# Kernel optimization log

Measured on AMD Instinct MI355X. Metric: run time of the kernel, lower is better.

Reference implementation:

```python
import jax, jax.numpy as jnp
import numpy as np

H = 512  # hidden_size


def setup_inputs() -> dict:
    key = jax.random.key(0)
    ks = jax.random.split(key, 8)
    B, L_tgt, L_src = 4, 32, 1024
    query = jax.random.normal(ks[0], (B, L_tgt, H), dtype=jnp.float32)
    states = jax.random.normal(ks[1], (B, L_src, 2 * H), dtype=jnp.float32)
    source_mask = jnp.ones((B, L_src), dtype=jnp.int32)
    s = 0.02
    Wq = jax.random.normal(ks[2], (H, 2 * H), dtype=jnp.float32) * s      # _linear_query.weight^T
    bq = jax.random.normal(ks[3], (2 * H,), dtype=jnp.float32) * s        # _linear_query.bias
    Ws = jax.random.normal(ks[4], (2 * H, 2 * H), dtype=jnp.float32) * s  # _linear_source.weight^T (no bias)
    v = jax.random.normal(ks[5], (2 * H,), dtype=jnp.float32) * s         # _v.weight (no bias)
    Wc = jax.random.normal(ks[6], (3 * H, H), dtype=jnp.float32) * s      # _context.weight^T
    bc = jax.random.normal(ks[7], (H,), dtype=jnp.float32) * s            # _context.bias
    return {"query": query, "states": states, "source_mask": source_mask,
            "Wq": Wq, "bq": bq, "Ws": Ws, "v": v, "Wc": Wc, "bc": bc}


def reference(query, states, source_mask, Wq, bq, Ws, v, Wc, bc):
    # Bahdanau additive attention.
    # query: (B, T, H), states: (B, S, 2H), source_mask: (B, S)
    qf = query @ Wq + bq                         # (B, T, 2H)
    sf = states @ Ws                             # (B, S, 2H)
    # alignments: v . tanh(qf[:, :, None] + sf[:, None, :])  -> (B, T, S)
    feats = jnp.tanh(qf[:, :, None, :] + sf[:, None, :, :])  # (B, T, S, 2H)
    alignments = jnp.einsum('btsd,d->bts', feats, v)
    # mask (B, S) -> (B, 1, S); masked positions get -inf before softmax
    alignments = jnp.where(source_mask[:, None, :].astype(bool), alignments, -jnp.inf)
    attentions = jax.nn.softmax(alignments, axis=2)           # (B, T, S)
    context = jnp.einsum('bts,bsd->btd', attentions, states)  # (B, T, 2H)
    concat_context = jnp.concatenate((context, query), axis=2)  # (B, T, 3H)
    attention_hidden = concat_context @ Wc + bc               # (B, T, H)
    attentions_t = jnp.swapaxes(attentions, 1, 2)             # (B, S, T)
    return (context, attention_hidden, attentions_t)
```

## Files before the change

### kernel.cpp

```cpp
#include <hip/hip_runtime.h>
#include <math.h>


typedef unsigned short u16;
typedef __bf16 bf16x8 __attribute__((ext_vector_type(8)));
typedef float floatx4 __attribute__((ext_vector_type(4)));

#define B_ 4
#define T_ 32
#define S_ 1024
#define H_ 512
#define D_ 1024
#define BT_ 128
#define TWO_LOG2E 2.8853900817779268f
#define LOG2E 1.4426950408889634f

__device__ __forceinline__ float bf2f(u16 u) {
  unsigned int i = ((unsigned int)u) << 16;
  return __builtin_bit_cast(float, i);
}
__device__ __forceinline__ u16 f2bf(float f) {
  unsigned int i = __builtin_bit_cast(unsigned int, f);
  i += 0x7fffu + ((i >> 16) & 1u);
  return (u16)(i >> 16);
}
__device__ __forceinline__ void ld_g2l_16(const u16* g, u16* l) {
  __builtin_amdgcn_global_load_lds((__attribute__((address_space(1))) void*)(u16*)g,
                                   (__attribute__((address_space(3))) void*)l, 16, 0, 0);
}


__global__ __launch_bounds__(256) void prep_fused6(const float* __restrict__ states, const float* __restrict__ Ws,
                                                   const float* __restrict__ query, const float* __restrict__ Wq,
                                                   const float* __restrict__ bq,
                                                   const float* __restrict__ Wc, const float* __restrict__ bc,
                                                   u16* __restrict__ sbf, u16* __restrict__ sbfT,
                                                   u16* __restrict__ WsT, float* __restrict__ qfp,
                                                   float* __restrict__ rowsum, float* __restrict__ hid) {
  __shared__ u16 tile[32][65];
  __shared__ float q[8][128];
  const int t = threadIdx.x;
  if (blockIdx.x < 256) {
    const int idx = blockIdx.x;
    const int c0 = (idx & 3) * 256, r0 = ((idx >> 2) & 15) * 8, ks = idx >> 6;
    const int k0 = ks * 128;
    for (int i = t; i < 8 * 128; i += 256) {
      const int rl = i >> 7, kk = i & 127;
      q[rl][kk] = query[(size_t)(r0 + rl) * H_ + k0 + kk];
    }
    __syncthreads();
    const int col = c0 + t;
    float acc[8] = {};
    for (int kk = 0; kk < 128; ++kk) {
      const float w = Wq[(size_t)(k0 + kk) * D_ + col];
#pragma unroll
      for (int r = 0; r < 8; ++r) acc[r] = fmaf(q[r][kk], w, acc[r]);
    }
    const float bb = (ks == 0) ? bq[col] : 0.f;
    float* dst = qfp + (size_t)ks * (BT_ * D_);
#pragma unroll
    for (int r = 0; r < 8; ++r)
      dst[(size_t)(r0 + r) * D_ + col] = TWO_LOG2E * (acc[r] + bb);
  } else if (blockIdx.x < 384) {
    const int idx = blockIdx.x - 256;
    const int c0 = (idx & 1) * 256, r0 = ((idx >> 1) & 15) * 8, ks = idx >> 5;
    const int k0 = ks * 128;
    for (int i = t; i < 8 * 128; i += 256) {
      const int rl = i >> 7, kk = i & 127;
      q[rl][kk] = query[(size_t)(r0 + rl) * H_ + k0 + kk];
    }
    __syncthreads();
    const int col = c0 + t;
    float acc[8] = {};
    for (int kk = 0; kk < 128; ++kk) {
      const float w = Wc[(size_t)(D_ + k0 + kk) * H_ + col];
#pragma unroll
      for (int r = 0; r < 8; ++r) acc[r] = fmaf(q[r][kk], w, acc[r]);
    }
    const float bb = (ks == 0) ? bc[col] : 0.f;
#pragma unroll
    for (int r = 0; r < 8; ++r)
      atomicAdd(&hid[(size_t)(r0 + r) * H_ + col], acc[r] + bb);
  } else if (blockIdx.x < 896) {
    const int bid = blockIdx.x - 384;
    if (bid == 0 && t < 128) rowsum[t] = 0.f;
    const int n0 = (bid & 15) * 64, k0 = (bid >> 4) * 32;
    const int kr = t >> 3, nc = (t & 7) * 8;
    const float* p = Ws + (size_t)(k0 + kr) * D_ + n0 + nc;
    float4 a = *(const float4*)p, b = *(const float4*)(p + 4);
    tile[kr][nc + 0] = f2bf(a.x); tile[kr][nc + 1] = f2bf(a.y);
    tile[kr][nc + 2] = f2bf(a.z); tile[kr][nc + 3] = f2bf(a.w);
    tile[kr][nc + 4] = f2bf(b.x); tile[kr][nc + 5] = f2bf(b.y);
    tile[kr][nc + 6] = f2bf(b.z); tile[kr][nc + 7] = f2bf(b.w);
    __syncthreads();
    const int nr = t >> 2, kc = (t & 3) * 8;
    union { uint4 v; u16 s[8]; } st;
#pragma unroll
    for (int i = 0; i < 8; ++i) st.s[i] = tile[kc + i][nr];
    *(uint4*)(WsT + (size_t)(n0 + nr) * D_ + k0 + kc) = st.v;
  } else {
    const int bid = blockIdx.x - 896;
    const int b = bid >> 9;
    const int r2 = bid & 511;
    const int d0 = (r2 & 15) * 64, s0 = (r2 >> 4) * 32;
    const int sr = t >> 3, dc = (t & 7) * 8;
    const float* p = states + ((size_t)b * S_ + s0 + sr) * D_ + d0 + dc;
    float4 a = *(const float4*)p, bb = *(const float4*)(p + 4);
    union { uint4 v; u16 s[8]; } pk;
    pk.s[0] = f2bf(a.x); pk.s[1] = f2bf(a.y); pk.s[2] = f2bf(a.z); pk.s[3] = f2bf(a.w);
    pk.s[4] = f2bf(bb.x); pk.s[5] = f2bf(bb.y); pk.s[6] = f2bf(bb.z); pk.s[7] = f2bf(bb.w);
    *(uint4*)(sbf + ((size_t)b * S_ + s0 + sr) * D_ + d0 + dc) = pk.v;
#pragma unroll
    for (int i = 0; i < 8; ++i) tile[sr][dc + i] = pk.s[i];
    __syncthreads();
    const int dr = t >> 2, sc = (t & 3) * 8;
    union { uint4 v; u16 s[8]; } st;
#pragma unroll
    for (int i = 0; i < 8; ++i) st.s[i] = tile[sc + i][dr];
    *(uint4*)(sbfT + ((size_t)b * D_ + d0 + dr) * S_ + s0 + sc) = st.v;
  }
}

__device__ __forceinline__ void f2f_stage(const u16* __restrict__ A, const u16* __restrict__ BT,
                                          u16* sAb, u16* sBb, int bm0, int bn0, int k0,
                                          int wv, int srow, int sp) {
#pragma unroll
  for (int j = 0; j < 4; ++j) {
    const int r = wv * 32 + j * 8 + srow;
    const int c = sp ^ (r & 7);
    ld_g2l_16(A + (size_t)(bm0 + r) * D_ + k0 + c * 8, sAb + (wv * 32 + j * 8) * 64);
  }
#pragma unroll
  for (int j = 0; j < 2; ++j) {
    const int r = wv * 16 + j * 8 + srow;
    const int c = sp ^ (r & 7);
    ld_g2l_16(BT + (size_t)(bn0 + r) * D_ + k0 + c * 8, sBb + (wv * 16 + j * 8) * 64);
  }
}

__device__ __forceinline__ void f2f_compute(const u16* sAb, const u16* sBb,
                                            int wm, int wn, int fm, int fq, floatx4 (&acc)[4][2]) {
#pragma unroll
  for (int win = 0; win < 2; ++win) {
    bf16x8 af[4], bfr[2];
#pragma unroll
    for (int i = 0; i < 4; ++i) {
      const int R = wm + i * 16 + fm;
      af[i] = *(const bf16x8*)&sAb[R * 64 + ((win * 4 + fq) ^ (R & 7)) * 8];
    }
#pragma unroll
    for (int j = 0; j < 2; ++j) {
      const int R = wn + j * 16 + fm;
      bfr[j] = *(const bf16x8*)&sBb[R * 64 + ((win * 4 + fq) ^ (R & 7)) * 8];
    }
#pragma unroll
    for (int i = 0; i < 4; ++i)
#pragma unroll
      for (int j = 0; j < 2; ++j)
        acc[i][j] = __builtin_amdgcn_mfma_f32_16x16x32_bf16(af[i], bfr[j], acc[i][j], 0, 0, 0);
  }
}

__global__ __launch_bounds__(256) void f2i_sfgemm(const u16* __restrict__ A, const u16* __restrict__ BT,
                                                  const float* __restrict__ qfp, float* __restrict__ Eq,
                                                  u16* __restrict__ Es) {
  __shared__ __align__(16) u16 sA[2][128 * 64];
  __shared__ __align__(16) u16 sB[2][64 * 64];
  const int bm0 = blockIdx.y * 128, bn0 = blockIdx.x * 64;
  const int t = threadIdx.x;
  const int wv = t >> 6, lane = t & 63;
  const int wm = (wv >> 1) * 64, wn = (wv & 1) * 32;
  const int fm = lane & 15, fq = lane >> 4;
  const int srow = lane >> 3, sp = lane & 7;

  {
    const int bid = blockIdx.y * 16 + blockIdx.x;
    const int idx = bid * 256 + t;
    const float s = qfp[idx] + qfp[BT_ * D_ + idx] +
                    qfp[2 * BT_ * D_ + idx] + qfp[3 * BT_ * D_ + idx];
    Eq[idx] = __builtin_amdgcn_exp2f(s);
  }

  floatx4 acc[4][2];
  const floatx4 fz = {0.f, 0.f, 0.f, 0.f};
#pragma unroll
  for (int i = 0; i < 4; ++i) { acc[i][0] = fz; acc[i][1] = fz; }

  f2f_stage(A, BT, sA[0], sB[0], bm0, bn0, 0, wv, srow, sp);
#pragma unroll 1
  for (int k0 = 0; k0 < D_; k0 += 128) {
    f2f_stage(A, BT, sA[1], sB[1], bm0, bn0, k0 + 64, wv, srow, sp);
    asm volatile("s_waitcnt vmcnt(6)" ::: "memory");
    __builtin_amdgcn_s_barrier();
    f2f_compute(sA[0], sB[0], wm, wn, fm, fq, acc);
    __builtin_amdgcn_s_barrier();
    if (k0 + 128 < D_) {
      f2f_stage(A, BT, sA[0], sB[0], bm0, bn0, k0 + 128, wv, srow, sp);
      asm volatile("s_waitcnt vmcnt(6)" ::: "memory");
    } else {
      asm volatile("s_waitcnt vmcnt(0)" ::: "memory");
    }
    __builtin_amdgcn_s_barrier();
    f2f_compute(sA[1], sB[1], wm, wn, fm, fq, acc);
    __builtin_amdgcn_s_barrier();
  }
#pragma unroll
  for (int i = 0; i < 4; ++i)
#pragma unroll
    for (int j = 0; j < 2; ++j)
#pragma unroll
      for (int r = 0; r < 4; ++r) {
        const int row = bm0 + wm + i * 16 + fq * 4 + r;
        const int col = bn0 + wn + j * 16 + fm;
        Es[(size_t)row * D_ + col] = f2bf(__builtin_amdgcn_exp2f(TWO_LOG2E * acc[i][j][r]));
      }
}

__global__ __launch_bounds__(256) void f3k_align(const float* __restrict__ Eq, const u16* __restrict__ Es,
                                                 const float* __restrict__ v, const int* __restrict__ mask,
                                                 u16* __restrict__ pbf, float* __restrict__ rowsum) {
  __shared__ float red[32][4];
  const int wv = threadIdx.x >> 6, lane = threadIdx.x & 63;
  const int w = blockIdx.x * 4 + wv;
  const int b = w >> 8;
  const int s0 = (w & 255) * 4;
  const int m0 = mask[(size_t)b * S_ + s0 + 0];
  const int m1 = mask[(size_t)b * S_ + s0 + 1];
  const int m2 = mask[(size_t)b * S_ + s0 + 2];
  const int m3 = mask[(size_t)b * S_ + s0 + 3];
  float vm2[16], es0[16], es1[16], es2[16], es3[16];
  float sumv = 0.f;
  {
    union { uint4 u[2]; u16 h[16]; } u0, u1, u2, u3;
    const uint4* ep0 = (const uint4*)(Es + ((size_t)b * S_ + s0 + 0) * D_ + lane * 16);
    const uint4* ep1 = (const uint4*)(Es + ((size_t)b * S_ + s0 + 1) * D_ + lane * 16);
    const uint4* ep2 = (const uint4*)(Es + ((size_t)b * S_ + s0 + 2) * D_ + lane * 16);
    const uint4* ep3 = (const uint4*)(Es + ((size_t)b * S_ + s0 + 3) * D_ + lane * 16);
    u0.u[0] = ep0[0]; u0.u[1] = ep0[1];
    u1.u[0] = ep1[0]; u1.u[1] = ep1[1];
    u2.u[0] = ep2[0]; u2.u[1] = ep2[1];
    u3.u[0] = ep3[0]; u3.u[1] = ep3[1];
    const float4* vp = (const float4*)(v + lane * 16);
#pragma unroll
    for (int c = 0; c < 4; ++c) {
      const float4 w4 = vp[c];
      vm2[4 * c + 0] = -2.f * w4.x; vm2[4 * c + 1] = -2.f * w4.y;
      vm2[4 * c + 2] = -2.f * w4.z; vm2[4 * c + 3] = -2.f * w4.w;
      sumv += w4.x + w4.y + w4.z + w4.w;
    }
#pragma unroll
    for (int j = 0; j < 16; ++j) {
      es0[j] = bf2f(u0.h[j]); es1[j] = bf2f(u1.h[j]);
      es2[j] = bf2f(u2.h[j]); es3[j] = bf2f(u3.h[j]);
    }
  }
  const float* qbase = Eq + ((size_t)(b * T_)) * D_ + lane * 16;
  for (int tc = 0; tc < 8; ++tc) {
    float sa[4], sb[4], sc[4], sd[4];
#pragma unroll
    for (int ti = 0; ti < 4; ++ti) {
      const float4* qp = (const float4*)(qbase + (size_t)(tc * 4 + ti) * D_);
      float a0 = sumv, a1 = sumv, a2 = sumv, a3 = sumv;
#pragma unroll
      for (int c = 0; c < 4; ++c) {
        const float4 q4 = qp[c];
        const float xs[4] = {q4.x, q4.y, q4.z, q4.w};
#pragma unroll
        for (int u2 = 0; u2 < 4; ++u2) {
          const int j = 4 * c + u2;
          a0 = fmaf(vm2[j], __builtin_amdgcn_rcpf(fmaf(xs[u2], es0[j], 1.f)), a0);
          a1 = fmaf(vm2[j], __builtin_amdgcn_rcpf(fmaf(xs[u2], es1[j], 1.f)), a1);
          a2 = fmaf(vm2[j], __builtin_amdgcn_rcpf(fmaf(xs[u2], es2[j], 1.f)), a2);
          a3 = fmaf(vm2[j], __builtin_amdgcn_rcpf(fmaf(xs[u2], es3[j], 1.f)), a3);
        }
      }
      sa[ti] = a0; sb[ti] = a1; sc[ti] = a2; sd[ti] = a3;
    }
#pragma unroll
    for (int off = 32; off > 0; off >>= 1)
#pragma unroll
      for (int ti = 0; ti < 4; ++ti) {
        sa[ti] += __shfl_xor(sa[ti], off);
        sb[ti] += __shfl_xor(sb[ti], off);
        sc[ti] += __shfl_xor(sc[ti], off);
        sd[ti] += __shfl_xor(sd[ti], off);
      }
    if (lane == 0) {
#pragma unroll
      for (int ti = 0; ti < 4; ++ti) {
        const int tt = tc * 4 + ti;
        const float e0 = m0 ? __builtin_amdgcn_exp2f(sa[ti] * LOG2E) : 0.f;
        const float e1 = m1 ? __builtin_amdgcn_exp2f(sb[ti] * LOG2E) : 0.f;
        const float e2 = m2 ? __builtin_amdgcn_exp2f(sc[ti] * LOG2E) : 0.f;
        const float e3 = m3 ? __builtin_amdgcn_exp2f(sd[ti] * LOG2E) : 0.f;
        const u16 p0 = f2bf(e0), p1 = f2bf(e1), p2 = f2bf(e2), p3 = f2bf(e3);
        uint2 pk;
        pk.x = (unsigned int)p0 | ((unsigned int)p1 << 16);
        pk.y = (unsigned int)p2 | ((unsigned int)p3 << 16);
        *(uint2*)&pbf[((size_t)(b * T_ + tt)) * S_ + s0] = pk;
        red[tt][wv] = bf2f(p0) + bf2f(p1) + bf2f(p2) + bf2f(p3);
      }
    }
  }
  __syncthreads();
  if (threadIdx.x < 32) {
    const int bb = blockIdx.x >> 6;
    const float rs = red[threadIdx.x][0] + red[threadIdx.x][1] +
                     red[threadIdx.x][2] + red[threadIdx.x][3];
    atomicAdd(&rowsum[bb * 32 + threadIdx.x], rs);
  }
}

__global__ __launch_bounds__(256) void f5e_context(const u16* __restrict__ pbf, const u16* __restrict__ sbfT,
                                                   const float* __restrict__ rowsum,
                                                   float* __restrict__ ctx, float* __restrict__ out_at) {
  __shared__ float rinv[32];
  __shared__ float red[4][64][9];
  const int b = blockIdx.x >> 6, dt = blockIdx.x & 63;
  const int wv = threadIdx.x >> 6, lane = threadIdx.x & 63;
  if (threadIdx.x < 32) rinv[threadIdx.x] = 1.f / rowsum[b * 32 + threadIdx.x];
  const int n0 = dt * 16;
  const int fm = lane & 15, fq = lane >> 4;
  const floatx4 fz = {0.f, 0.f, 0.f, 0.f};
  floatx4 acc0 = fz, acc1 = fz;
  const u16* pa0 = pbf + ((size_t)b * T_ + fm) * S_ + wv * 256 + fq * 8;
  const u16* pa1 = pa0 + (size_t)16 * S_;
  const u16* pb  = sbfT + ((size_t)b * D_ + n0 + fm) * S_ + wv * 256 + fq * 8;
#pragma unroll
  for (int k0 = 0; k0 < 256; k0 += 32) {
    bf16x8 a0 = *(const bf16x8*)(pa0 + k0);
    bf16x8 a1 = *(const bf16x8*)(pa1 + k0);
    bf16x8 bb = *(const bf16x8*)(pb + k0);
    acc0 = __builtin_amdgcn_mfma_f32_16x16x32_bf16(a0, bb, acc0, 0, 0, 0);
    acc1 = __builtin_amdgcn_mfma_f32_16x16x32_bf16(a1, bb, acc1, 0, 0, 0);
  }
#pragma unroll
  for (int r = 0; r < 4; ++r) {
    red[wv][lane][r] = acc0[r];
    red[wv][lane][4 + r] = acc1[r];
  }
  __syncthreads();
  const int s0a = dt * 16;
  for (int i = threadIdx.x; i < 512; i += 256) {
    const int tt = i & 31, sl = i >> 5;
    const float e = bf2f(pbf[((size_t)(b * T_ + tt)) * S_ + s0a + sl]);
    out_at[((size_t)(b * S_ + s0a + sl)) * T_ + tt] = e * rinv[tt];
  }
  if (wv == 0) {
#pragma unroll
    for (int r = 0; r < 4; ++r) {
      const float v0 = red[0][lane][r] + red[1][lane][r] + red[2][lane][r] + red[3][lane][r];
      const float v1 = red[0][lane][4 + r] + red[1][lane][4 + r] +
                       red[2][lane][4 + r] + red[3][lane][4 + r];
      const int t0r = fq * 4 + r;
      ctx[((size_t)b * T_ + t0r) * D_ + n0 + fm] = v0 * rinv[t0r];
      ctx[((size_t)b * T_ + 16 + t0r) * D_ + n0 + fm] = v1 * rinv[16 + t0r];
    }
  }
}

__global__ __launch_bounds__(256) void f6c_outproj(const float* __restrict__ ctx,
                                                   const float* __restrict__ Wc,
                                                   float* __restrict__ out_hid) {
  __shared__ float cq[16][128];
  const int c0 = blockIdx.x * 128, r0 = blockIdx.y * 16, k0 = blockIdx.z * 128;
  const int tid = threadIdx.x;
  const int cl = tid & 127, rh = tid >> 7;
  for (int i = tid; i < 16 * 128; i += 256) {
    const int rl = i >> 7, kk = i & 127;
    cq[rl][kk] = ctx[(size_t)(r0 + rl) * D_ + k0 + kk];
  }
  __syncthreads();
  float acc[8] = {};
  for (int kk = 0; kk < 128; ++kk) {
    const float w = Wc[(size_t)(k0 + kk) * H_ + c0 + cl];
#pragma unroll
    for (int rr = 0; rr < 8; ++rr) acc[rr] = fmaf(cq[rh * 8 + rr][kk], w, acc[rr]);
  }
#pragma unroll
  for (int rr = 0; rr < 8; ++rr)
    atomicAdd(&out_hid[(size_t)(r0 + rh * 8 + rr) * H_ + c0 + cl], acc[rr]);
}


__global__ __launch_bounds__(256) void prep_fused(const float* __restrict__ states, const float* __restrict__ Ws,
                                                  const float* __restrict__ query, const float* __restrict__ Wq,
                                                  const float* __restrict__ bq,
                                                  u16* __restrict__ sbf, u16* __restrict__ sbfT,
                                                  u16* __restrict__ WsT, float* __restrict__ qf) {
  __shared__ u16 tile[32][65];
  __shared__ float q[8][128];
  const int t = threadIdx.x;
  if (blockIdx.x < 512) {
    const int n0 = (blockIdx.x & 15) * 64, k0 = (blockIdx.x >> 4) * 32;
    const int kr = t >> 3, nc = (t & 7) * 8;
    const float* p = Ws + (size_t)(k0 + kr) * D_ + n0 + nc;
    float4 a = *(const float4*)p, b = *(const float4*)(p + 4);
    tile[kr][nc + 0] = f2bf(a.x); tile[kr][nc + 1] = f2bf(a.y);
    tile[kr][nc + 2] = f2bf(a.z); tile[kr][nc + 3] = f2bf(a.w);
    tile[kr][nc + 4] = f2bf(b.x); tile[kr][nc + 5] = f2bf(b.y);
    tile[kr][nc + 6] = f2bf(b.z); tile[kr][nc + 7] = f2bf(b.w);
    __syncthreads();
    const int nr = t >> 2, kc = (t & 3) * 8;
    union { uint4 v; u16 s[8]; } st;
#pragma unroll
    for (int i = 0; i < 8; ++i) st.s[i] = tile[kc + i][nr];
    *(uint4*)(WsT + (size_t)(n0 + nr) * D_ + k0 + kc) = st.v;
  } else if (blockIdx.x < 2560) {
    const int bid = blockIdx.x - 512;
    const int b = bid >> 9;
    const int r2 = bid & 511;
    const int d0 = (r2 & 15) * 64, s0 = (r2 >> 4) * 32;
    const int sr = t >> 3, dc = (t & 7) * 8;
    const float* p = states + ((size_t)b * S_ + s0 + sr) * D_ + d0 + dc;
    float4 a = *(const float4*)p, bb = *(const float4*)(p + 4);
    union { uint4 v; u16 s[8]; } pk;
    pk.s[0] = f2bf(a.x); pk.s[1] = f2bf(a.y); pk.s[2] = f2bf(a.z); pk.s[3] = f2bf(a.w);
    pk.s[4] = f2bf(bb.x); pk.s[5] = f2bf(bb.y); pk.s[6] = f2bf(bb.z); pk.s[7] = f2bf(bb.w);
    *(uint4*)(sbf + ((size_t)b * S_ + s0 + sr) * D_ + d0 + dc) = pk.v;
#pragma unroll
    for (int i = 0; i < 8; ++i) tile[sr][dc + i] = pk.s[i];
    __syncthreads();
    const int dr = t >> 2, sc = (t & 3) * 8;
    union { uint4 v; u16 s[8]; } st;
#pragma unroll
    for (int i = 0; i < 8; ++i) st.s[i] = tile[sc + i][dr];
    *(uint4*)(sbfT + ((size_t)b * D_ + d0 + dr) * S_ + s0 + sc) = st.v;
  } else {
    const int idx = blockIdx.x - 2560;
    const int c0 = (idx & 3) * 256, r0 = ((idx >> 2) & 15) * 8, k0 = (idx >> 6) * 128;
    for (int i = t; i < 8 * 128; i += 256) {
      const int rl = i >> 7, kk = i & 127;
      q[rl][kk] = query[(size_t)(r0 + rl) * H_ + k0 + kk];
    }
    __syncthreads();
    const int col = c0 + t;
    float acc[8] = {};
    for (int kk = 0; kk < 128; ++kk) {
      const float w = Wq[(size_t)(k0 + kk) * D_ + col];
#pragma unroll
      for (int r = 0; r < 8; ++r) acc[r] = fmaf(q[r][kk], w, acc[r]);
    }
    const float bb = (k0 == 0) ? bq[col] : 0.f;
#pragma unroll
    for (int r = 0; r < 8; ++r)
      atomicAdd(&qf[(size_t)(r0 + r) * D_ + col], TWO_LOG2E * (acc[r] + bb));
  }
}

__global__ __launch_bounds__(256) void f2e_sfgemm(const u16* __restrict__ A, const u16* __restrict__ BT,
                                                  u16* __restrict__ Cb) {
  __shared__ __align__(16) u16 sA[128 * 64];
  __shared__ __align__(16) u16 sB[64 * 64];
  const int bm0 = blockIdx.y * 128, bn0 = blockIdx.x * 64;
  const int t = threadIdx.x;
  const int wv = t >> 6, lane = t & 63;
  const int wm = (wv >> 1) * 64, wn = (wv & 1) * 32;
  const int fm = lane & 15, fq = lane >> 4;
  const int srow = lane >> 3, sp = lane & 7;

  floatx4 acc[4][2];
  const floatx4 fz = {0.f, 0.f, 0.f, 0.f};
#pragma unroll
  for (int i = 0; i < 4; ++i) { acc[i][0] = fz; acc[i][1] = fz; }

  for (int k0 = 0; k0 < D_; k0 += 64) {
    __syncthreads();
#pragma unroll
    for (int j = 0; j < 4; ++j) {
      const int r = wv * 32 + j * 8 + srow;
      const int c = sp ^ (r & 7);
      ld_g2l_16(A + (size_t)(bm0 + r) * D_ + k0 + c * 8, &sA[(wv * 32 + j * 8) * 64]);
    }
#pragma unroll
    for (int j = 0; j < 2; ++j) {
      const int r = wv * 16 + j * 8 + srow;
      const int c = sp ^ (r & 7);
      ld_g2l_16(BT + (size_t)(bn0 + r) * D_ + k0 + c * 8, &sB[(wv * 16 + j * 8) * 64]);
    }
    __syncthreads();
#pragma unroll
    for (int win = 0; win < 2; ++win) {
      bf16x8 af[4], bfr[2];
#pragma unroll
      for (int i = 0; i < 4; ++i) {
        const int R = wm + i * 16 + fm;
        af[i] = *(const bf16x8*)&sA[R * 64 + ((win * 4 + fq) ^ (R & 7)) * 8];
      }
#pragma unroll
      for (int j = 0; j < 2; ++j) {
        const int R = wn + j * 16 + fm;
        bfr[j] = *(const bf16x8*)&sB[R * 64 + ((win * 4 + fq) ^ (R & 7)) * 8];
      }
#pragma unroll
      for (int i = 0; i < 4; ++i)
#pragma unroll
        for (int j = 0; j < 2; ++j)
          acc[i][j] = __builtin_amdgcn_mfma_f32_16x16x32_bf16(af[i], bfr[j], acc[i][j], 0, 0, 0);
    }
  }
#pragma unroll
  for (int i = 0; i < 4; ++i)
#pragma unroll
    for (int j = 0; j < 2; ++j)
#pragma unroll
      for (int r = 0; r < 4; ++r) {
        const int row = bm0 + wm + i * 16 + fq * 4 + r;
        const int col = bn0 + wn + j * 16 + fm;
        Cb[(size_t)row * D_ + col] = f2bf(TWO_LOG2E * acc[i][j][r]);
      }
}

__global__ __launch_bounds__(256, 6) void f3f_align(const float* __restrict__ qf, const u16* __restrict__ sfb,
                                                    const float* __restrict__ v, float* __restrict__ alg) {
  const int wid = (blockIdx.x * 256 + threadIdx.x) >> 6;
  const int lane = threadIdx.x & 63;
  const int b = wid >> 10, s = wid & 1023;
  const int t0 = blockIdx.y * 16;
  float vr[16], sr[16];
  {
    union { uint4 v[2]; u16 s[16]; } u;
    const uint4* sp = (const uint4*)(sfb + (size_t)wid * D_ + lane * 16);
    u.v[0] = sp[0]; u.v[1] = sp[1];
    const float* vp = v + lane * 16;
#pragma unroll
    for (int c = 0; c < 4; ++c) {
      float4 w = *(const float4*)(vp + 4 * c);
      vr[4 * c + 0] = w.x; vr[4 * c + 1] = w.y; vr[4 * c + 2] = w.z; vr[4 * c + 3] = w.w;
    }
#pragma unroll
    for (int j = 0; j < 16; ++j) sr[j] = bf2f(u.s[j]);
  }
  float sum[16];
#pragma unroll
  for (int tt = 0; tt < 16; ++tt) sum[tt] = 0.f;

  const float* qbase = qf + ((size_t)(b * T_ + t0)) * D_ + lane * 16;
  for (int tt = 0; tt < 16; ++tt) {
    const float4* qp = (const float4*)(qbase + (size_t)tt * D_);
    float acc = 0.f;
#pragma unroll
    for (int c = 0; c < 4; ++c) {
      float4 q4 = qp[c];
      float xs[4] = {q4.x, q4.y, q4.z, q4.w};
#pragma unroll
      for (int u2 = 0; u2 < 4; ++u2) {
        const int j = 4 * c + u2;
        const float x = xs[u2] + sr[j];
        const float e = __builtin_amdgcn_exp2f(x);
        acc = fmaf(vr[j], fmaf(-2.f, __builtin_amdgcn_rcpf(e + 1.f), 1.f), acc);
      }
    }
    sum[tt] = acc;
  }
#pragma unroll
  for (int off = 32; off > 0; off >>= 1)
#pragma unroll
    for (int tt = 0; tt < 16; ++tt) sum[tt] += __shfl_xor(sum[tt], off);
  if (lane == 0) {
#pragma unroll
    for (int tt = 0; tt < 16; ++tt)
      alg[((size_t)(b * T_ + t0 + tt)) * S_ + s] = sum[tt];
  }
}

__global__ __launch_bounds__(256) void f4b_softmax(const float* __restrict__ alg, const int* __restrict__ mask,
                                                   float* __restrict__ out_at, u16* __restrict__ pbf) {
  const int r = blockIdx.x;
  const int b = r >> 5, t = r & 31;
  const int tid = threadIdx.x;
  __shared__ float red[256];
  float a[4];
#pragma unroll
  for (int jj = 0; jj < 4; ++jj) {
    const int s = tid + 256 * jj;
    const float x = alg[(size_t)r * S_ + s];
    a[jj] = (mask[(size_t)b * S_ + s] != 0) ? x : -3.0e38f;
  }
  float m = fmaxf(fmaxf(a[0], a[1]), fmaxf(a[2], a[3]));
  red[tid] = m; __syncthreads();
  for (int st = 128; st > 0; st >>= 1) { if (tid < st) red[tid] = fmaxf(red[tid], red[tid + st]); __syncthreads(); }
  m = red[0]; __syncthreads();
  float e[4], lsum = 0.f;
#pragma unroll
  for (int jj = 0; jj < 4; ++jj) {
    e[jj] = (a[jj] > -1.0e38f) ? expf(a[jj] - m) : 0.f;
    lsum += e[jj];
  }
  red[tid] = lsum; __syncthreads();
  for (int st = 128; st > 0; st >>= 1) { if (tid < st) red[tid] += red[tid + st]; __syncthreads(); }
  const float rs = 1.f / red[0];
#pragma unroll
  for (int jj = 0; jj < 4; ++jj) {
    const int s = tid + 256 * jj;
    const float p = e[jj] * rs;
    out_at[((size_t)b * S_ + s) * T_ + t] = p;
    pbf[(size_t)r * S_ + s] = f2bf(p);
  }
}

__global__ __launch_bounds__(256) void f5c_context(const u16* __restrict__ pbf, const u16* __restrict__ sbfT,
                                                   float* __restrict__ ctx) {
  const int b = blockIdx.x >> 4, dt = blockIdx.x & 15;
  const int wv = threadIdx.x >> 6, lane = threadIdx.x & 63;
  const int n0 = dt * 64 + wv * 16;
  const int fm = lane & 15, fq = lane >> 4;
  const floatx4 fz = {0.f, 0.f, 0.f, 0.f};
  floatx4 acc0 = fz, acc1 = fz;
  const u16* pa0 = pbf + ((size_t)b * T_ + fm) * S_ + fq * 8;
  const u16* pa1 = pbf + ((size_t)b * T_ + 16 + fm) * S_ + fq * 8;
  const u16* pb  = sbfT + ((size_t)b * D_ + n0 + fm) * S_ + fq * 8;
#pragma unroll 4
  for (int k0 = 0; k0 < S_; k0 += 32) {
    bf16x8 a0 = *(const bf16x8*)(pa0 + k0);
    bf16x8 a1 = *(const bf16x8*)(pa1 + k0);
    bf16x8 bb = *(const bf16x8*)(pb + k0);
    acc0 = __builtin_amdgcn_mfma_f32_16x16x32_bf16(a0, bb, acc0, 0, 0, 0);
    acc1 = __builtin_amdgcn_mfma_f32_16x16x32_bf16(a1, bb, acc1, 0, 0, 0);
  }
  const int col = n0 + fm;
#pragma unroll
  for (int r = 0; r < 4; ++r) {
    ctx[((size_t)b * T_ + fq * 4 + r) * D_ + col] = acc0[r];
    ctx[((size_t)b * T_ + 16 + fq * 4 + r) * D_ + col] = acc1[r];
  }
}

__global__ __launch_bounds__(256) void f6b_outproj(const float* __restrict__ ctx, const float* __restrict__ query,
                                                   const float* __restrict__ Wc, const float* __restrict__ bc,
                                                   float* __restrict__ out_hid) {
  __shared__ float cq[16][128];
  const int c0 = blockIdx.x * 128, r0 = blockIdx.y * 16, k0 = blockIdx.z * 128;
  const int tid = threadIdx.x;
  const int cl = tid & 127, rh = tid >> 7;
  for (int i = tid; i < 16 * 128; i += 256) {
    const int rl = i >> 7, kk = i & 127;
    const int k = k0 + kk, row = r0 + rl;
    cq[rl][kk] = (k < D_) ? ctx[(size_t)row * D_ + k] : query[(size_t)row * H_ + k - D_];
  }
  __syncthreads();
  float acc[8] = {};
  for (int kk = 0; kk < 128; ++kk) {
    const float w = Wc[(size_t)(k0 + kk) * H_ + c0 + cl];
#pragma unroll
    for (int rr = 0; rr < 8; ++rr) acc[rr] = fmaf(cq[rh * 8 + rr][kk], w, acc[rr]);
  }
  const float bb = (blockIdx.z == 0) ? bc[c0 + cl] : 0.f;
#pragma unroll
  for (int rr = 0; rr < 8; ++rr)
    atomicAdd(&out_hid[(size_t)(r0 + rh * 8 + rr) * H_ + c0 + cl], acc[rr] + bb);
}


__global__ __launch_bounds__(256) void kc_cvt(const float* __restrict__ in, u16* __restrict__ out) {
  const size_t i0 = ((size_t)blockIdx.x * 256 + threadIdx.x) * 8;
  float4 a = *(const float4*)(in + i0);
  float4 b = *(const float4*)(in + i0 + 4);
  union { uint4 v; u16 s[8]; } r;
  r.s[0] = f2bf(a.x); r.s[1] = f2bf(a.y); r.s[2] = f2bf(a.z); r.s[3] = f2bf(a.w);
  r.s[4] = f2bf(b.x); r.s[5] = f2bf(b.y); r.s[6] = f2bf(b.z); r.s[7] = f2bf(b.w);
  *(uint4*)(out + i0) = r.v;
}

__global__ __launch_bounds__(256) void f0_transpose(const float* __restrict__ Ws, u16* __restrict__ WsT) {
  __shared__ u16 tile[32][65];
  const int n0 = blockIdx.x * 64, k0 = blockIdx.y * 32;
  const int t = threadIdx.x;
  {
    const int kr = t >> 3, nc = (t & 7) * 8;
    const float* p = Ws + (size_t)(k0 + kr) * D_ + n0 + nc;
    float4 a = *(const float4*)p, b = *(const float4*)(p + 4);
    tile[kr][nc + 0] = f2bf(a.x); tile[kr][nc + 1] = f2bf(a.y);
    tile[kr][nc + 2] = f2bf(a.z); tile[kr][nc + 3] = f2bf(a.w);
    tile[kr][nc + 4] = f2bf(b.x); tile[kr][nc + 5] = f2bf(b.y);
    tile[kr][nc + 6] = f2bf(b.z); tile[kr][nc + 7] = f2bf(b.w);
  }
  __syncthreads();
  {
    const int nr = t >> 2, kc = (t & 3) * 8;
    union { uint4 v; u16 s[8]; } st;
#pragma unroll
    for (int i = 0; i < 8; ++i) st.s[i] = tile[kc + i][nr];
    *(uint4*)(WsT + (size_t)(n0 + nr) * D_ + k0 + kc) = st.v;
  }
}

__global__ __launch_bounds__(256) void f1b_qf(const float* __restrict__ query, const float* __restrict__ Wq,
                                              const float* __restrict__ bq, float* __restrict__ qf) {
  __shared__ float q[8][128];
  const int c0 = blockIdx.x * 256, r0 = blockIdx.y * 8, k0 = blockIdx.z * 128;
  const int tid = threadIdx.x;
  for (int i = tid; i < 8 * 128; i += 256) {
    const int rl = i >> 7, kk = i & 127;
    q[rl][kk] = query[(size_t)(r0 + rl) * H_ + k0 + kk];
  }
  __syncthreads();
  const int col = c0 + tid;
  float acc[8] = {};
  for (int kk = 0; kk < 128; ++kk) {
    const float w = Wq[(size_t)(k0 + kk) * D_ + col];
#pragma unroll
    for (int r = 0; r < 8; ++r) acc[r] = fmaf(q[r][kk], w, acc[r]);
  }
  const float bb = (blockIdx.z == 0) ? bq[col] : 0.f;
#pragma unroll
  for (int r = 0; r < 8; ++r)
    atomicAdd(&qf[(size_t)(r0 + r) * D_ + col], TWO_LOG2E * (acc[r] + bb));
}

__global__ __launch_bounds__(256) void f2c_sfgemm(const u16* __restrict__ A, const u16* __restrict__ BT,
                                                  u16* __restrict__ Cb) {
  __shared__ __align__(16) u16 sA[128 * 40];
  __shared__ __align__(16) u16 sB[64 * 40];
  const int bm0 = blockIdx.y * 128, bn0 = blockIdx.x * 64;
  const int t = threadIdx.x;
  const int wv = t >> 6, lane = t & 63;
  const int wm = (wv >> 1) * 64, wn = (wv & 1) * 32;
  const int fm = lane & 15, fq = lane >> 4;
  const int arow = t >> 1, akc = (t & 1) * 16;
  const int brow = t >> 2, bkc = (t & 3) * 8;
  floatx4 acc[4][2];
  const floatx4 fz = {0.f, 0.f, 0.f, 0.f};
#pragma unroll
  for (int i = 0; i < 4; ++i) { acc[i][0] = fz; acc[i][1] = fz; }
  const uint4* gA = (const uint4*)(A + (size_t)(bm0 + arow) * D_ + akc);
  const uint4* gB = (const uint4*)(BT + (size_t)(bn0 + brow) * D_ + bkc);
  for (int k0 = 0; k0 < D_; k0 += 32) {
    uint4 va0 = gA[k0 >> 3];
    uint4 va1 = gA[(k0 >> 3) + 1];
    uint4 vb = gB[k0 >> 3];
    __syncthreads();
    *(uint4*)&sA[arow * 40 + akc] = va0;
    *(uint4*)&sA[arow * 40 + akc + 8] = va1;
    *(uint4*)&sB[brow * 40 + bkc] = vb;
    __syncthreads();
    bf16x8 af[4], bfr[2];
#pragma unroll
    for (int i = 0; i < 4; ++i) af[i] = *(const bf16x8*)&sA[(wm + i * 16 + fm) * 40 + fq * 8];
#pragma unroll
    for (int j = 0; j < 2; ++j) bfr[j] = *(const bf16x8*)&sB[(wn + j * 16 + fm) * 40 + fq * 8];
#pragma unroll
    for (int i = 0; i < 4; ++i)
#pragma unroll
      for (int j = 0; j < 2; ++j)
        acc[i][j] = __builtin_amdgcn_mfma_f32_16x16x32_bf16(af[i], bfr[j], acc[i][j], 0, 0, 0);
  }
#pragma unroll
  for (int i = 0; i < 4; ++i)
#pragma unroll
    for (int j = 0; j < 2; ++j)
#pragma unroll
      for (int r = 0; r < 4; ++r) {
        const int row = bm0 + wm + i * 16 + fq * 4 + r;
        const int col = bn0 + wn + j * 16 + fm;
        Cb[(size_t)row * D_ + col] = f2bf(TWO_LOG2E * acc[i][j][r]);
      }
}

__global__ __launch_bounds__(256) void f2d_sfgemm(const float* __restrict__ A, const u16* __restrict__ BT,
                                                  u16* __restrict__ Cb) {
  __shared__ __align__(16) u16 sA[128 * 40];
  __shared__ __align__(16) u16 sB[64 * 40];
  const int bm0 = blockIdx.y * 128, bn0 = blockIdx.x * 64;
  const int t = threadIdx.x;
  const int wv = t >> 6, lane = t & 63;
  const int wm = (wv >> 1) * 64, wn = (wv & 1) * 32;
  const int fm = lane & 15, fq = lane >> 4;
  const int arow = t >> 1, akc = (t & 1) * 16;
  const int brow = t >> 2, bkc = (t & 3) * 8;
  floatx4 acc[4][2];
  const floatx4 fz = {0.f, 0.f, 0.f, 0.f};
#pragma unroll
  for (int i = 0; i < 4; ++i) { acc[i][0] = fz; acc[i][1] = fz; }
  const float* gA = A + (size_t)(bm0 + arow) * D_ + akc;
  const uint4* gB = (const uint4*)(BT + (size_t)(bn0 + brow) * D_ + bkc);
  for (int k0 = 0; k0 < D_; k0 += 32) {
    float4 a0 = *(const float4*)(gA + k0);
    float4 a1 = *(const float4*)(gA + k0 + 4);
    float4 a2 = *(const float4*)(gA + k0 + 8);
    float4 a3 = *(const float4*)(gA + k0 + 12);
    uint4 vb = gB[k0 >> 3];
    union { uint4 v[2]; u16 s[16]; } pa;
    pa.s[0] = f2bf(a0.x); pa.s[1] = f2bf(a0.y); pa.s[2] = f2bf(a0.z); pa.s[3] = f2bf(a0.w);
    pa.s[4] = f2bf(a1.x); pa.s[5] = f2bf(a1.y); pa.s[6] = f2bf(a1.z); pa.s[7] = f2bf(a1.w);
    pa.s[8] = f2bf(a2.x); pa.s[9] = f2bf(a2.y); pa.s[10] = f2bf(a2.z); pa.s[11] = f2bf(a2.w);
    pa.s[12] = f2bf(a3.x); pa.s[13] = f2bf(a3.y); pa.s[14] = f2bf(a3.z); pa.s[15] = f2bf(a3.w);
    __syncthreads();
    *(uint4*)&sA[arow * 40 + akc] = pa.v[0];
    *(uint4*)&sA[arow * 40 + akc + 8] = pa.v[1];
    *(uint4*)&sB[brow * 40 + bkc] = vb;
    __syncthreads();
    bf16x8 af[4], bfr[2];
#pragma unroll
    for (int i = 0; i < 4; ++i) af[i] = *(const bf16x8*)&sA[(wm + i * 16 + fm) * 40 + fq * 8];
#pragma unroll
    for (int j = 0; j < 2; ++j) bfr[j] = *(const bf16x8*)&sB[(wn + j * 16 + fm) * 40 + fq * 8];
#pragma unroll
    for (int i = 0; i < 4; ++i)
#pragma unroll
      for (int j = 0; j < 2; ++j)
        acc[i][j] = __builtin_amdgcn_mfma_f32_16x16x32_bf16(af[i], bfr[j], acc[i][j], 0, 0, 0);
  }
#pragma unroll
  for (int i = 0; i < 4; ++i)
#pragma unroll
    for (int j = 0; j < 2; ++j)
#pragma unroll
      for (int r = 0; r < 4; ++r) {
        const int row = bm0 + wm + i * 16 + fq * 4 + r;
        const int col = bn0 + wn + j * 16 + fm;
        Cb[(size_t)row * D_ + col] = f2bf(TWO_LOG2E * acc[i][j][r]);
      }
}

__global__ __launch_bounds__(256) void f4_softmax(const float* __restrict__ alg, const int* __restrict__ mask,
                                                  float* __restrict__ attn) {
  const int r = blockIdx.x;
  const int b = r >> 5;
  const int tid = threadIdx.x;
  __shared__ float red[256];
  float a[4];
#pragma unroll
  for (int jj = 0; jj < 4; ++jj) {
    const int s = tid + 256 * jj;
    const float x = alg[(size_t)r * S_ + s];
    a[jj] = (mask[(size_t)b * S_ + s] != 0) ? x : -3.0e38f;
  }
  float m = fmaxf(fmaxf(a[0], a[1]), fmaxf(a[2], a[3]));
  red[tid] = m; __syncthreads();
  for (int st = 128; st > 0; st >>= 1) { if (tid < st) red[tid] = fmaxf(red[tid], red[tid + st]); __syncthreads(); }
  m = red[0]; __syncthreads();
  float e[4], lsum = 0.f;
#pragma unroll
  for (int jj = 0; jj < 4; ++jj) {
    e[jj] = (a[jj] > -1.0e38f) ? expf(a[jj] - m) : 0.f;
    lsum += e[jj];
  }
  red[tid] = lsum; __syncthreads();
  for (int st = 128; st > 0; st >>= 1) { if (tid < st) red[tid] += red[tid + st]; __syncthreads(); }
  const float rs = 1.f / red[0];
#pragma unroll
  for (int jj = 0; jj < 4; ++jj)
    attn[(size_t)r * S_ + tid + 256 * jj] = e[jj] * rs;
}

__global__ __launch_bounds__(256) void f5b_context(const float* __restrict__ attn, const u16* __restrict__ sbf,
                                                   float* __restrict__ ctx, float* __restrict__ out_at) {
  __shared__ float at[16][64];
  const int s0 = blockIdx.x * 64, t0 = blockIdx.y * 16, b = blockIdx.z;
  const int tid = threadIdx.x;
  for (int i = tid; i < 16 * 64; i += 256) {
    const int tl = i >> 6, sl = i & 63;
    at[tl][sl] = attn[(size_t)(b * T_ + t0 + tl) * S_ + s0 + sl];
  }
  __syncthreads();
  for (int i = tid; i < 64 * 16; i += 256) {
    const int sl = i >> 4, tl = i & 15;
    out_at[((size_t)b * S_ + s0 + sl) * T_ + t0 + tl] = at[tl][sl];
  }
  float acc[16][4] = {};
  for (int sl = 0; sl < 64; ++sl) {
    const u16* srow = sbf + ((size_t)b * S_ + s0 + sl) * D_ + tid;
    float sv[4];
#pragma unroll
    for (int jj = 0; jj < 4; ++jj) sv[jj] = bf2f(srow[256 * jj]);
#pragma unroll
    for (int tl = 0; tl < 16; ++tl) {
      const float w = at[tl][sl];
#pragma unroll
      for (int jj = 0; jj < 4; ++jj) acc[tl][jj] = fmaf(w, sv[jj], acc[tl][jj]);
    }
  }
#pragma unroll
  for (int tl = 0; tl < 16; ++tl)
#pragma unroll
    for (int jj = 0; jj < 4; ++jj)
      atomicAdd(&ctx[(size_t)(b * T_ + t0 + tl) * D_ + tid + 256 * jj], acc[tl][jj]);
}

__global__ __launch_bounds__(256) void f5_context(const float* __restrict__ attn, const float* __restrict__ states,
                                                  float* __restrict__ ctx, float* __restrict__ out_at) {
  __shared__ float at[16][64];
  const int s0 = blockIdx.x * 64, t0 = blockIdx.y * 16, b = blockIdx.z;
  const int tid = threadIdx.x;
  for (int i = tid; i < 16 * 64; i += 256) {
    const int tl = i >> 6, sl = i & 63;
    at[tl][sl] = attn[(size_t)(b * T_ + t0 + tl) * S_ + s0 + sl];
  }
  __syncthreads();
  for (int i = tid; i < 64 * 16; i += 256) {
    const int sl = i >> 4, tl = i & 15;
    out_at[((size_t)b * S_ + s0 + sl) * T_ + t0 + tl] = at[tl][sl];
  }
  float acc[16][4] = {};
  for (int sl = 0; sl < 64; ++sl) {
    const float* srow = states + ((size_t)b * S_ + s0 + sl) * D_ + tid;
    float sv[4];
#pragma unroll
    for (int jj = 0; jj < 4; ++jj) sv[jj] = srow[256 * jj];
#pragma unroll
    for (int tl = 0; tl < 16; ++tl) {
      const float w = at[tl][sl];
#pragma unroll
      for (int jj = 0; jj < 4; ++jj) acc[tl][jj] = fmaf(w, sv[jj], acc[tl][jj]);
    }
  }
#pragma unroll
  for (int tl = 0; tl < 16; ++tl)
#pragma unroll
    for (int jj = 0; jj < 4; ++jj)
      atomicAdd(&ctx[(size_t)(b * T_ + t0 + tl) * D_ + tid + 256 * jj], acc[tl][jj]);
}


__global__ __launch_bounds__(256) void k1_qf(const float* __restrict__ query, const float* __restrict__ Wq,
                                             const float* __restrict__ bq, float* __restrict__ qf) {
  const int r = blockIdx.x;
  const int tid = threadIdx.x;
  __shared__ float q[H_];
  for (int i = tid; i < H_; i += 256) q[i] = query[(size_t)r * H_ + i];
  __syncthreads();
#pragma unroll
  for (int jj = 0; jj < 4; ++jj) {
    const int j = tid + 256 * jj;
    float acc = bq[j];
    for (int k = 0; k < H_; ++k) acc = fmaf(q[k], Wq[(size_t)k * D_ + j], acc);
    qf[(size_t)r * D_ + j] = acc;
  }
}

__global__ __launch_bounds__(256) void k23_align(const float* __restrict__ states, const float* __restrict__ Ws,
                                                 const float* __restrict__ v, const float* __restrict__ qf,
                                                 float* __restrict__ alg) {
  const int b = blockIdx.x >> 6;
  const int s0 = (blockIdx.x & 63) * 16;
  const int tid = threadIdx.x, lane = tid & 63, wv = tid >> 6;
  __shared__ u16 stL[16 * D_];
  __shared__ float vvL[D_];
  __shared__ float red[16 * 4];
  for (int i = tid; i < 16 * D_; i += 256) {
    const int row = i >> 10, col = i & (D_ - 1);
    stL[i] = f2bf(states[((size_t)b * S_ + s0 + row) * D_ + col]);
  }
  for (int i = tid; i < D_; i += 256) vvL[i] = v[i];
  __syncthreads();
  float acc[64];
#pragma unroll
  for (int i = 0; i < 64; ++i) acc[i] = 0.f;
#pragma unroll 4
  for (int k = 0; k < D_; ++k) {
    float wsv[4];
#pragma unroll
    for (int jj = 0; jj < 4; ++jj) wsv[jj] = Ws[(size_t)k * D_ + tid + 256 * jj];
#pragma unroll
    for (int i = 0; i < 16; ++i) {
      const float sv = bf2f(stL[i * D_ + k]);
#pragma unroll
      for (int jj = 0; jj < 4; ++jj) acc[i * 4 + jj] = fmaf(sv, wsv[jj], acc[i * 4 + jj]);
    }
  }
  for (int t = 0; t < T_; ++t) {
    float qv[4];
#pragma unroll
    for (int jj = 0; jj < 4; ++jj) qv[jj] = qf[((size_t)b * T_ + t) * D_ + tid + 256 * jj];
    float part[16];
#pragma unroll
    for (int i = 0; i < 16; ++i) {
      float p = 0.f;
#pragma unroll
      for (int jj = 0; jj < 4; ++jj)
        p = fmaf(vvL[tid + 256 * jj], tanhf(qv[jj] + acc[i * 4 + jj]), p);
      part[i] = p;
    }
#pragma unroll
    for (int i = 0; i < 16; ++i) {
      float x = part[i];
#pragma unroll
      for (int off = 32; off > 0; off >>= 1) x += __shfl_xor(x, off);
      if (lane == 0) red[i * 4 + wv] = x;
    }
    __syncthreads();
    if (tid < 16)
      alg[((size_t)b * T_ + t) * S_ + s0 + tid] =
          red[tid * 4 + 0] + red[tid * 4 + 1] + red[tid * 4 + 2] + red[tid * 4 + 3];
    __syncthreads();
  }
}

__global__ __launch_bounds__(256) void k4_softmax(const float* __restrict__ alg, const int* __restrict__ mask,
                                                  float* __restrict__ attn) {
  const int r = blockIdx.x;
  const int b = r >> 5;
  const int tid = threadIdx.x;
  __shared__ float red[256];
  float a[4];
#pragma unroll
  for (int jj = 0; jj < 4; ++jj) {
    const int s = tid + 256 * jj;
    const float x = alg[(size_t)r * S_ + s];
    a[jj] = (mask[(size_t)b * S_ + s] != 0) ? x : -3.0e38f;
  }
  float m = fmaxf(fmaxf(a[0], a[1]), fmaxf(a[2], a[3]));
  red[tid] = m; __syncthreads();
  for (int st = 128; st > 0; st >>= 1) { if (tid < st) red[tid] = fmaxf(red[tid], red[tid + st]); __syncthreads(); }
  m = red[0]; __syncthreads();
  float e[4], lsum = 0.f;
#pragma unroll
  for (int jj = 0; jj < 4; ++jj) {
    e[jj] = (a[jj] > -1.0e38f) ? expf(a[jj] - m) : 0.f;
    lsum += e[jj];
  }
  red[tid] = lsum; __syncthreads();
  for (int st = 128; st > 0; st >>= 1) { if (tid < st) red[tid] += red[tid + st]; __syncthreads(); }
  const float rs = 1.f / red[0];
#pragma unroll
  for (int jj = 0; jj < 4; ++jj)
    attn[(size_t)r * S_ + tid + 256 * jj] = e[jj] * rs;
}

__global__ __launch_bounds__(256) void k56_ctx_proj(const float* __restrict__ attn, const float* __restrict__ states,
                                                    const float* __restrict__ query, const float* __restrict__ Wc,
                                                    const float* __restrict__ bc,
                                                    float* __restrict__ out_ctx, float* __restrict__ out_hid,
                                                    float* __restrict__ out_at) {
  const int r = blockIdx.x;
  const int b = r >> 5, t = r & (T_ - 1);
  const int tid = threadIdx.x;
  __shared__ float pr[S_];
  __shared__ float cq[D_ + H_];
  for (int s = tid; s < S_; s += 256) pr[s] = attn[(size_t)r * S_ + s];
  __syncthreads();
  for (int s = tid; s < S_; s += 256) out_at[((size_t)b * S_ + s) * T_ + t] = pr[s];
  float acc[4] = {0.f, 0.f, 0.f, 0.f};
  for (int s = 0; s < S_; ++s) {
    const float w = pr[s];
    const float* srow = states + ((size_t)b * S_ + s) * D_ + tid;
#pragma unroll
    for (int jj = 0; jj < 4; ++jj) acc[jj] = fmaf(w, srow[256 * jj], acc[jj]);
  }
#pragma unroll
  for (int jj = 0; jj < 4; ++jj) {
    cq[tid + 256 * jj] = acc[jj];
    out_ctx[(size_t)r * D_ + tid + 256 * jj] = acc[jj];
  }
  for (int i = tid; i < H_; i += 256) cq[D_ + i] = query[(size_t)r * H_ + i];
  __syncthreads();
#pragma unroll
  for (int jj = 0; jj < 2; ++jj) {
    const int n = tid + 256 * jj;
    float h = bc[n];
    for (int k = 0; k < D_ + H_; ++k) h = fmaf(cq[k], Wc[(size_t)k * H_ + n], h);
    out_hid[(size_t)r * H_ + n] = h;
  }
}

extern "C" void kernel_launch(void* const* d_in, const int* in_sizes, int n_in,
                              void* d_out, int out_size, void* d_ws, size_t ws_size,
                              hipStream_t stream) {
  const float* query  = (const float*)d_in[0];
  const float* states = (const float*)d_in[1];
  const int*   mask   = (const int*)d_in[2];
  const float* Wq     = (const float*)d_in[3];
  const float* bq     = (const float*)d_in[4];
  const float* Ws     = (const float*)d_in[5];
  const float* v      = (const float*)d_in[6];
  const float* Wc     = (const float*)d_in[7];
  const float* bc     = (const float*)d_in[8];

  float* A  = (float*)d_out;
  float* Bh = A + (size_t)BT_ * D_;
  float* C  = Bh + (size_t)BT_ * H_;

  char* ws = (char*)d_ws;
  u16*   sfb  = (u16*)(ws + 0);
  u16*   WsT  = (u16*)(ws + 8388608);
  float* alg  = (float*)(ws + 10485760);
  u16*   sbf  = (u16*)(ws + 11010048);
  u16*   sbfT = (u16*)(ws + 19398656);
  u16*   pbf  = (u16*)(ws + 27787264);

  const size_t WS_T1 = 11010048;
  const size_t WS_T2 = 19398656;
  const size_t WS_T3 = 28049408;
  const size_t WS_T4 = 36962816;

  if (ws_size >= WS_T4) {
    float* qfp  = (float*)(ws + 0);
    u16*   Es16 = (u16*)(ws + 28049408);
    float* Eq4  = (float*)(ws + 36438016);
    float* rsum = (float*)(ws + 36962304);
    (void)hipMemsetAsync(Bh, 0, (size_t)BT_ * H_ * 4, stream);
    prep_fused6<<<2944, 256, 0, stream>>>(states, Ws, query, Wq, bq, Wc, bc,
                                          sbf, sbfT, WsT, qfp, rsum, Bh);
    f2i_sfgemm<<<dim3(16, 32), 256, 0, stream>>>(sbf, WsT, qfp, Eq4, Es16);
    f3k_align<<<256, 256, 0, stream>>>(Eq4, Es16, v, mask, pbf, rsum);
    f5e_context<<<256, 256, 0, stream>>>(pbf, sbfT, rsum, A, C);
    f6c_outproj<<<dim3(4, 8, 8), 256, 0, stream>>>(A, Wc, Bh);
  } else if (ws_size >= WS_T3) {
    (void)hipMemsetAsync(A, 0, (size_t)(BT_ * D_ + BT_ * H_) * 4, stream);
    prep_fused<<<2816, 256, 0, stream>>>(states, Ws, query, Wq, bq, sbf, sbfT, WsT, A);
    f2e_sfgemm<<<dim3(16, 32), 256, 0, stream>>>(sbf, WsT, sfb);
    f3f_align<<<dim3(1024, 2), 256, 0, stream>>>(A, sfb, v, alg);
    f4b_softmax<<<BT_, 256, 0, stream>>>(alg, mask, C, pbf);
    f5c_context<<<64, 256, 0, stream>>>(pbf, sbfT, A);
    f6b_outproj<<<dim3(4, 8, 12), 256, 0, stream>>>(A, query, Wc, bc, Bh);
  } else if (ws_size >= WS_T1) {
    float* attn = alg;
    (void)hipMemsetAsync(A, 0, (size_t)(BT_ * D_ + BT_ * H_) * 4, stream);
    f1b_qf<<<dim3(4, 16, 4), 256, 0, stream>>>(query, Wq, bq, A);
    f0_transpose<<<dim3(16, 32), 256, 0, stream>>>(Ws, WsT);
    const int tier2 = (ws_size >= WS_T2);
    if (tier2) {
      kc_cvt<<<2048, 256, 0, stream>>>(states, sbf);
      f2c_sfgemm<<<dim3(16, 32), 256, 0, stream>>>(sbf, WsT, sfb);
    } else {
      f2d_sfgemm<<<dim3(16, 32), 256, 0, stream>>>(states, WsT, sfb);
    }
    f3f_align<<<dim3(1024, 2), 256, 0, stream>>>(A, sfb, v, C);
    (void)hipMemsetAsync(A, 0, (size_t)BT_ * D_ * 4, stream);
    f4_softmax<<<BT_, 256, 0, stream>>>(C, mask, attn);
    if (tier2)
      f5b_context<<<dim3(16, 2, 4), 256, 0, stream>>>(attn, sbf, A, C);
    else
      f5_context<<<dim3(16, 2, 4), 256, 0, stream>>>(attn, states, A, C);
    f6b_outproj<<<dim3(4, 8, 12), 256, 0, stream>>>(A, query, Wc, bc, Bh);
  } else {
    k1_qf<<<BT_, 256, 0, stream>>>(query, Wq, bq, A);
    k23_align<<<B_ * (S_ / 16), 256, 0, stream>>>(states, Ws, v, A, C);
    k4_softmax<<<BT_, 256, 0, stream>>>(C, mask, A);
    k56_ctx_proj<<<BT_, 256, 0, stream>>>(A, states, query, Wc, bc, A, Bh, C);
  }
}
```

Baseline: 165.3 us.

## Reduce split-K partials in-block for query projections, drop memset and partial buffer

The query projections (Wq and the query part of Wc) now split K across the four waves of a block and reduce the partials through shared memory, instead of using separate split-K blocks. The Wq path applies bias and exp2 in place and writes Eq directly. The Wc path writes hid with plain stores, which removes the memset and the atomics. The sfgemm kernel no longer reads four partial buffers to build Eq. In exchange, each block loads the full query rows into shared memory and performs an extra shared-memory reduction.

```diff
diff --git a/kernel.cpp b/kernel.cpp
--- a/kernel.cpp
+++ b/kernel.cpp
@@ -30,58 +30,63 @@
 }
 
 
-__global__ __launch_bounds__(256) void prep_fused6(const float* __restrict__ states, const float* __restrict__ Ws,
+__global__ __launch_bounds__(256) void prep_fused7(const float* __restrict__ states, const float* __restrict__ Ws,
                                                    const float* __restrict__ query, const float* __restrict__ Wq,
                                                    const float* __restrict__ bq,
                                                    const float* __restrict__ Wc, const float* __restrict__ bc,
                                                    u16* __restrict__ sbf, u16* __restrict__ sbfT,
-                                                   u16* __restrict__ WsT, float* __restrict__ qfp,
+                                                   u16* __restrict__ WsT, float* __restrict__ Eq,
                                                    float* __restrict__ rowsum, float* __restrict__ hid) {
-  __shared__ u16 tile[32][65];
-  __shared__ float q[8][128];
+  __shared__ __align__(16) float smem[4096];
   const int t = threadIdx.x;
-  if (blockIdx.x < 256) {
-    const int idx = blockIdx.x;
-    const int c0 = (idx & 3) * 256, r0 = ((idx >> 2) & 15) * 8, ks = idx >> 6;
-    const int k0 = ks * 128;
-    for (int i = t; i < 8 * 128; i += 256) {
-      const int rl = i >> 7, kk = i & 127;
-      q[rl][kk] = query[(size_t)(r0 + rl) * H_ + k0 + kk];
-    }
-    __syncthreads();
-    const int col = c0 + t;
+  if (blockIdx.x < 384) {
+    const int isQ = (blockIdx.x < 256);
+    const int idx = isQ ? blockIdx.x : blockIdx.x - 256;
+    const int c0 = isQ ? (idx & 15) * 64 : (idx & 7) * 64;
+    const int r0 = isQ ? (idx >> 4) * 8 : (idx >> 3) * 8;
+    float* qq = smem;
+    const float4* qsrc = (const float4*)(query + (size_t)r0 * H_);
+    for (int i = t; i < 1024; i += 256) ((float4*)qq)[i] = qsrc[i];
+    __syncthreads();
+    const int kg = t >> 6, cl = t & 63;
+    const int col = c0 + cl;
+    const int kbase = kg * 128;
     float acc[8] = {};
-    for (int kk = 0; kk < 128; ++kk) {
-      const float w = Wq[(size_t)(k0 + kk) * D_ + col];
-#pragma unroll
-      for (int r = 0; r < 8; ++r) acc[r] = fmaf(q[r][kk], w, acc[r]);
-    }
-    const float bb = (ks == 0) ? bq[col] : 0.f;
-    float* dst = qfp + (size_t)ks * (BT_ * D_);
-#pragma unroll
-    for (int r = 0; r < 8; ++r)
-      dst[(size_t)(r0 + r) * D_ + col] = TWO_LOG2E * (acc[r] + bb);
-  } else if (blockIdx.x < 384) {
-    const int idx = blockIdx.x - 256;
-    const int c0 = (idx & 1) * 256, r0 = ((idx >> 1) & 15) * 8, ks = idx >> 5;
-    const int k0 = ks * 128;
-    for (int i = t; i < 8 * 128; i += 256) {
-      const int rl = i >> 7, kk = i & 127;
-      q[rl][kk] = query[(size_t)(r0 + rl) * H_ + k0 + kk];
-    }
-    __syncthreads();
-    const int col = c0 + t;
-    float acc[8] = {};
-    for (int kk = 0; kk < 128; ++kk) {
-      const float w = Wc[(size_t)(D_ + k0 + kk) * H_ + col];
-#pragma unroll
-      for (int r = 0; r < 8; ++r) acc[r] = fmaf(q[r][kk], w, acc[r]);
-    }
-    const float bb = (ks == 0) ? bc[col] : 0.f;
-#pragma unroll
-    for (int r = 0; r < 8; ++r)
-      atomicAdd(&hid[(size_t)(r0 + r) * H_ + col], acc[r] + bb);
+    if (isQ) {
+      for (int kk = 0; kk < 128; ++kk) {
+        const float w = Wq[(size_t)(kbase + kk) * D_ + col];
+#pragma unroll
+        for (int r = 0; r < 8; ++r) acc[r] = fmaf(qq[r * 512 + kbase + kk], w, acc[r]);
+      }
+    } else {
+      for (int kk = 0; kk < 128; ++kk) {
+        const float w = Wc[(size_t)(D_ + kbase + kk) * H_ + col];
+#pragma unroll
+        for (int r = 0; r < 8; ++r) acc[r] = fmaf(qq[r * 512 + kbase + kk], w, acc[r]);
+      }
+    }
+    __syncthreads();
+    float* red = smem;
+#pragma unroll
+    for (int r = 0; r < 8; ++r) red[(kg * 8 + r) * 64 + cl] = acc[r];
+    __syncthreads();
+    if (isQ) {
+      for (int o = t; o < 512; o += 256) {
+        const int r = o >> 6, c = o & 63;
+        const float s = red[(0 * 8 + r) * 64 + c] + red[(1 * 8 + r) * 64 + c] +
+                        red[(2 * 8 + r) * 64 + c] + red[(3 * 8 + r) * 64 + c] + bq[c0 + c];
+        Eq[(size_t)(r0 + r) * D_ + c0 + c] = __builtin_amdgcn_exp2f(TWO_LOG2E * s);
+      }
+    } else {
+      for (int o = t; o < 512; o += 256) {
+        const int r = o >> 6, c = o & 63;
+        const float s = red[(0 * 8 + r) * 64 + c] + red[(1 * 8 + r) * 64 + c] +
+                        red[(2 * 8 + r) * 64 + c] + red[(3 * 8 + r) * 64 + c] + bc[c0 + c];
+        hid[(size_t)(r0 + r) * H_ + c0 + c] = s;
+      }
+    }
   } else if (blockIdx.x < 896) {
+    u16 (*tile)[65] = (u16(*)[65])smem;
     const int bid = blockIdx.x - 384;
     if (bid == 0 && t < 128) rowsum[t] = 0.f;
     const int n0 = (bid & 15) * 64, k0 = (bid >> 4) * 32;
@@ -99,6 +104,7 @@
     for (int i = 0; i < 8; ++i) st.s[i] = tile[kc + i][nr];
     *(uint4*)(WsT + (size_t)(n0 + nr) * D_ + k0 + kc) = st.v;
   } else {
+    u16 (*tile)[65] = (u16(*)[65])smem;
     const int bid = blockIdx.x - 896;
     const int b = bid >> 9;
     const int r2 = bid & 511;
@@ -161,8 +167,7 @@
   }
 }
 
-__global__ __launch_bounds__(256) void f2i_sfgemm(const u16* __restrict__ A, const u16* __restrict__ BT,
-                                                  const float* __restrict__ qfp, float* __restrict__ Eq,
+__global__ __launch_bounds__(256) void f2j_sfgemm(const u16* __restrict__ A, const u16* __restrict__ BT,
                                                   u16* __restrict__ Es) {
   __shared__ __align__(16) u16 sA[2][128 * 64];
   __shared__ __align__(16) u16 sB[2][64 * 64];
@@ -172,14 +177,6 @@
   const int wm = (wv >> 1) * 64, wn = (wv & 1) * 32;
   const int fm = lane & 15, fq = lane >> 4;
   const int srow = lane >> 3, sp = lane & 7;
-
-  {
-    const int bid = blockIdx.y * 16 + blockIdx.x;
-    const int idx = bid * 256 + t;
-    const float s = qfp[idx] + qfp[BT_ * D_ + idx] +
-                    qfp[2 * BT_ * D_ + idx] + qfp[3 * BT_ * D_ + idx];
-    Eq[idx] = __builtin_amdgcn_exp2f(s);
-  }
 
   floatx4 acc[4][2];
   const floatx4 fz = {0.f, 0.f, 0.f, 0.f};
@@ -1085,14 +1082,12 @@
   const size_t WS_T4 = 36962816;
 
   if (ws_size >= WS_T4) {
-    float* qfp  = (float*)(ws + 0);
     u16*   Es16 = (u16*)(ws + 28049408);
     float* Eq4  = (float*)(ws + 36438016);
     float* rsum = (float*)(ws + 36962304);
-    (void)hipMemsetAsync(Bh, 0, (size_t)BT_ * H_ * 4, stream);
-    prep_fused6<<<2944, 256, 0, stream>>>(states, Ws, query, Wq, bq, Wc, bc,
-                                          sbf, sbfT, WsT, qfp, rsum, Bh);
-    f2i_sfgemm<<<dim3(16, 32), 256, 0, stream>>>(sbf, WsT, qfp, Eq4, Es16);
+    prep_fused7<<<2944, 256, 0, stream>>>(states, Ws, query, Wq, bq, Wc, bc,
+                                          sbf, sbfT, WsT, Eq4, rsum, Bh);
+    f2j_sfgemm<<<dim3(16, 32), 256, 0, stream>>>(sbf, WsT, Es16);
     f3k_align<<<256, 256, 0, stream>>>(Eq4, Es16, v, mask, pbf, rsum);
     f5e_context<<<256, 256, 0, stream>>>(pbf, sbfT, rsum, A, C);
     f6c_outproj<<<dim3(4, 8, 8), 256, 0, stream>>>(A, Wc, Bh);
```

Result: slower. 184.2 us (+11.4%).
